# Kernel tuning notes

Measured on AMD Instinct MI355X. Metric: run time of the kernel, lower is better.

The kernel has to match this reference:

```python
import jax, jax.numpy as jnp
import numpy as np

N, K, DIM = 65536, 32, 64


def setup_inputs() -> dict:
    key = jax.random.key(0)
    k1, k2, k3, k4 = jax.random.split(key, 4)
    x = jax.random.normal(k1, (N, DIM), jnp.float32)
    log_pi = jax.random.normal(k2, (K, 1), jnp.float32)
    mu = jax.random.normal(k3, (K, DIM), jnp.float32)
    log_sigma_ = jax.random.normal(k4, (K, DIM, DIM), jnp.float32) / 100.0
    return {"x": x, "log_pi": log_pi, "mu": mu, "log_sigma_": log_sigma_}


def reference(x, log_pi, mu, log_sigma_):
    k, d = mu.shape
    # Faithful to torch: softmax over the size-1 last axis of (K,1) -> all ones.
    pi = jax.nn.softmax(log_pi, axis=-1)  # (K, 1)
    # scale_tril construction: strict lower triangle kept, diagonal -> exp(diag) + 1e-3
    diag = jnp.exp(jnp.diagonal(log_sigma_, axis1=-2, axis2=-1)) + 1e-3  # (K, d)
    L = jnp.tril(log_sigma_, -1) + jnp.eye(d, dtype=x.dtype) * diag[:, None, :]  # (K, d, d)
    # batched MVN log_prob via triangular solve
    diff = x[:, None, :] - mu[None, :, :]            # (N, K, d)
    b = jnp.transpose(diff, (1, 2, 0))               # (K, d, N)
    z = jax.scipy.linalg.solve_triangular(L, b, lower=True)  # (K, d, N)
    maha = jnp.sum(z * z, axis=1)                    # (K, N)
    logdet = jnp.sum(jnp.log(diag), axis=-1)         # (K,)
    logp = -0.5 * (maha + d * jnp.log(2.0 * jnp.pi)) - logdet[:, None]  # (K, N)
    p = jnp.exp(logp).T                              # (N, K)
    return jnp.log(jnp.matmul(p, pi).squeeze())      # (N,)
```

## Files before the change

### kernel.cpp

```cpp
#include <hip/hip_runtime.h>

#define KK 32
#define DD 64
#define NB 65536
#define PAD 68
#define FRAGS 6
#define SLOT (FRAGS * 64)
#define MREF 103.0f
#define L2E 1.4426950408889634f

typedef __attribute__((ext_vector_type(8))) short bf16x8;
typedef __attribute__((ext_vector_type(4))) float f32x4;

__device__ inline short f2bf(float f) {
  uint32_t u = __builtin_bit_cast(uint32_t, f);
  uint32_t r = (u + 0x7fffu + ((u >> 16) & 1u)) >> 16;
  return (short)(r & 0xffffu);
}
__device__ inline uint4 pack8(const short* v) {
  uint4 u;
  u.x = (uint32_t)(unsigned short)v[0] | ((uint32_t)(unsigned short)v[1] << 16);
  u.y = (uint32_t)(unsigned short)v[2] | ((uint32_t)(unsigned short)v[3] << 16);
  u.z = (uint32_t)(unsigned short)v[4] | ((uint32_t)(unsigned short)v[5] << 16);
  u.w = (uint32_t)(unsigned short)v[6] | ((uint32_t)(unsigned short)v[7] << 16);
  return u;
}

__device__ __forceinline__ void gl_lds16(const uint4* g, uint4* l) {
  __builtin_amdgcn_global_load_lds(
      (__attribute__((address_space(1))) void*)g,
      (__attribute__((address_space(3))) void*)l, 16, 0, 0);
}

__global__ __launch_bounds__(256) void md_prep(const float* __restrict__ ls,
                                               const float* __restrict__ mu,
                                               uint4* __restrict__ Bp,
                                               float* __restrict__ Cc,
                                               float* __restrict__ Kcl2) {
  __shared__ float Ls[DD * DD];
  __shared__ float Ys[DD * PAD];
  __shared__ float invdL[DD];
  __shared__ float muL[DD];
  const int k = blockIdx.x, t = threadIdx.x;
  const int j = t >> 2, sub = t & 3;
  const float* __restrict__ lsk = ls + (size_t)k * DD * DD;

#pragma unroll
  for (int it = 0; it < 4; ++it) {
    const int o = (it * 256 + t) * 4;
    *(float4*)&Ls[o] = *(const float4*)&lsk[o];
  }
  if (t < DD) muL[t] = mu[k * DD + t];
  __syncthreads();
  if (t < DD) invdL[t] = 1.0f / (expf(Ls[t * DD + t]) + 1e-3f);
  __syncthreads();

  const float invdj = invdL[j];
  float z[16];
#pragma unroll
  for (int mi = 0; mi < 16; ++mi) z[mi] = 0.f;
#pragma unroll
  for (int i = 0; i < DD; ++i) {
    float p = 0.f;
#pragma unroll
    for (int mi = 0; mi < 16; ++mi) {
      if (4 * mi < i) {
        const int m = 4 * mi + sub;
        p = fmaf(Ls[i * DD + m], (m < i) ? z[mi] : 0.f, p);
      }
    }
    p += __shfl_xor(p, 1, 64);
    p += __shfl_xor(p, 2, 64);
    const float zi = (i == j) ? invdj : -p * invdL[i];
    if (sub == (i & 3)) z[i >> 2] = zi;
  }
#pragma unroll
  for (int mi = 0; mi < 16; ++mi) Ys[(4 * mi + sub) * PAD + j] = z[mi];
  __syncthreads();

  {
    float p = 0.f;
#pragma unroll
    for (int mi = 0; mi < 16; ++mi) {
      const int m = 4 * mi + sub;
      p = fmaf(Ys[j * PAD + m], muL[m], p);
    }
    p += __shfl_xor(p, 1, 64);
    p += __shfl_xor(p, 2, 64);
    if (sub == 0) Cc[k * DD + j] = p;
  }

  if (t < DD) {
    float r = -logf(invdL[t]);
#pragma unroll
    for (int off = 32; off > 0; off >>= 1) r += __shfl_down(r, off, 64);
    if (t == 0)
      Kcl2[k] = (MREF - 0.5f * (64.0f * 1.83787706640934534f) - r) * L2E;
  }

  if (t < DD) {
    const int colp = t & 15, qp = t >> 4;
    uint4* slot = Bp + (size_t)k * SLOT;
#pragma unroll
    for (int s = 0; s < 2; ++s) {
#pragma unroll
      for (int ct = 0; ct < 4; ++ct) {
        if (s == 1 && ct < 2) continue;
        const int i = colp + 16 * ct;
        short hh[8];
#pragma unroll
        for (int jj = 0; jj < 8; ++jj) {
          const int m = s * 32 + qp * 8 + jj;
          const float v = Ys[i * PAD + m] - ((i == m) ? 1.0f : 0.0f);
          hh[jj] = f2bf(v);
        }
        const int fi = (s == 0) ? ct : (2 + ct);
        slot[fi * 64 + t] = pack8(hh);
      }
    }
  }
}

__global__ __launch_bounds__(256, 2) void md_main(const float* __restrict__ x,
                                                  const uint4* __restrict__ Bp,
                                                  const float* __restrict__ Cc,
                                                  const float* __restrict__ Kcl2,
                                                  float* __restrict__ P) {
  __shared__ uint4 lds4[2 * SLOT];
  __shared__ float CcL[8 * DD];
  const int tid = threadIdx.x, lane = tid & 63, w = tid >> 6;
  const int quarter = blockIdx.x & 3;
  const int sblk = blockIdx.x >> 2;
  const int base = sblk * 256 + w * 64;
  const int k0 = quarter * 8;
  const int col = lane & 15, q = lane >> 4;

  bf16x8 Xh[4][2];
#pragma unroll
  for (int Bt = 0; Bt < 4; ++Bt) {
#pragma unroll
    for (int s = 0; s < 2; ++s) {
      const float* src = x + (size_t)(base + Bt * 16 + col) * DD + s * 32 + q * 8;
      const float4 v0 = *(const float4*)src;
      const float4 v1 = *(const float4*)(src + 4);
      const float f[8] = {v0.x, v0.y, v0.z, v0.w, v1.x, v1.y, v1.z, v1.w};
      bf16x8 h;
#pragma unroll
      for (int jj = 0; jj < 8; ++jj) h[jj] = f2bf(f[jj]);
      Xh[Bt][s] = h;
    }
  }

  f32x4 xg[4][4];
#pragma unroll
  for (int ct = 0; ct < 4; ++ct)
#pragma unroll
    for (int Bt = 0; Bt < 4; ++Bt)
      xg[ct][Bt] = *(const f32x4*)&x[(size_t)(base + Bt * 16 + col) * DD +
                                     ct * 16 + q * 4];

  CcL[tid] = Cc[k0 * DD + tid];
  CcL[256 + tid] = Cc[k0 * DD + 256 + tid];

  const int nfr = (w < 2) ? 2 : 1;
  const int fr0 = (w < 2) ? 2 * w : (2 + w);

  {
    const uint4* src = Bp + (size_t)k0 * SLOT;
#pragma unroll
    for (int it = 0; it < 2; ++it)
      if (it < nfr)
        gl_lds16(src + (fr0 + it) * 64 + lane, &lds4[(fr0 + it) * 64]);
  }
  __syncthreads();

  float run_s[4] = {0.f, 0.f, 0.f, 0.f};

#pragma unroll
  for (int kk = 0; kk < 8; ++kk) {
    const int k = k0 + kk;
    const int p = kk & 1;
    if (kk < 7) {
      const uint4* src = Bp + (size_t)(k + 1) * SLOT;
#pragma unroll
      for (int it = 0; it < 2; ++it)
        if (it < nfr)
          gl_lds16(src + (fr0 + it) * 64 + lane,
                   &lds4[(1 - p) * SLOT + (fr0 + it) * 64]);
    }
    const float kc = Kcl2[k];

    const uint4* buf = &lds4[p * SLOT];
    f32x4 mah[4];
#pragma unroll
    for (int Bt = 0; Bt < 4; ++Bt) mah[Bt] = (f32x4){0.f, 0.f, 0.f, 0.f};

#pragma unroll
    for (int ct = 0; ct < 4; ++ct) {
      const bf16x8 A0 = *(const bf16x8*)&buf[ct * 64 + lane];
      bf16x8 A1{};
      if (ct >= 2) A1 = *(const bf16x8*)&buf[(2 + ct) * 64 + lane];
      const f32x4 cK = *(const f32x4*)&CcL[kk * DD + ct * 16 + q * 4];
#pragma unroll
      for (int Bt = 0; Bt < 4; ++Bt) {
        f32x4 z = xg[ct][Bt];
        z = __builtin_amdgcn_mfma_f32_16x16x32_bf16(A0, Xh[Bt][0], z, 0, 0, 0);
        if (ct >= 2)
          z = __builtin_amdgcn_mfma_f32_16x16x32_bf16(A1, Xh[Bt][1], z, 0, 0, 0);
        const f32x4 d = z - cK;
        mah[Bt] += d * d;
      }
    }

#pragma unroll
    for (int Bt = 0; Bt < 4; ++Bt) {
      float s = (mah[Bt][0] + mah[Bt][1]) + (mah[Bt][2] + mah[Bt][3]);
      s += __shfl_xor(s, 16, 64);
      s += __shfl_xor(s, 32, 64);
      const float tt = fmaf(-0.5f * L2E, s, kc);
      run_s[Bt] += exp2f(tt);
    }

    if (kk < 7) __syncthreads();
  }

  if (q == 0) {
#pragma unroll
    for (int Bt = 0; Bt < 4; ++Bt) {
      const int sid = base + Bt * 16 + col;
      P[quarter * NB + sid] = run_s[Bt];
    }
  }
}

__global__ __launch_bounds__(256) void md_comb(const float* __restrict__ P,
                                               float* __restrict__ out) {
  const int n = blockIdx.x * 256 + threadIdx.x;
  const float S = (P[n] + P[NB + n]) + (P[2 * NB + n] + P[3 * NB + n]);
  out[n] = logf(S) - MREF;
}

extern "C" void kernel_launch(void* const* d_in, const int* in_sizes, int n_in,
                              void* d_out, int out_size, void* d_ws, size_t ws_size,
                              hipStream_t stream) {
  const float* x  = (const float*)d_in[0];
  const float* mu = (const float*)d_in[2];
  const float* ls = (const float*)d_in[3];
  float* out = (float*)d_out;

  char* ws = (char*)d_ws;
  uint4* Bp   = (uint4*)ws;
  float* P    = (float*)(ws + (size_t)KK * SLOT * 16);
  float* Cc   = P + 4 * NB;
  float* Kcl2 = Cc + KK * DD;

  md_prep<<<KK, 256, 0, stream>>>(ls, mu, Bp, Cc, Kcl2);
  md_main<<<1024, 256, 0, stream>>>(x, Bp, Cc, Kcl2, P);
  md_comb<<<NB / 256, 256, 0, stream>>>(P, out);
}
```

Baseline: 111.1 us.

## Split mixture components across two blocks and stage two components per barrier

Each md_main block now handles 16 mixture components instead of 8, so the grid shrinks from 1024 to 512 blocks. The x tile is therefore loaded and converted to bf16 half as often, and the partial-sum buffer and combine kernel shrink from four slices to two. The B-matrix prefetch now stages two components per double-buffer step, halving the number of __syncthreads per block. In exchange each block uses twice the LDS, and only 512 blocks are launched, which may reduce occupancy and latency hiding across the device's CUs.

Result: faster. 104.6 us (-5.9%).

```diff
diff --git a/kernel.cpp b/kernel.cpp
--- a/kernel.cpp
+++ b/kernel.cpp
@@ -126,13 +126,13 @@
                                                   const float* __restrict__ Cc,
                                                   const float* __restrict__ Kcl2,
                                                   float* __restrict__ P) {
-  __shared__ uint4 lds4[2 * SLOT];
-  __shared__ float CcL[8 * DD];
+  __shared__ uint4 lds4[4 * SLOT];
+  __shared__ float CcL[16 * DD];
   const int tid = threadIdx.x, lane = tid & 63, w = tid >> 6;
-  const int quarter = blockIdx.x & 3;
-  const int sblk = blockIdx.x >> 2;
+  const int half = blockIdx.x & 1;
+  const int sblk = blockIdx.x >> 1;
   const int base = sblk * 256 + w * 64;
-  const int k0 = quarter * 8;
+  const int k0 = half * 16;
   const int col = lane & 15, q = lane >> 4;
 
   bf16x8 Xh[4][2];
@@ -159,76 +159,78 @@
       xg[ct][Bt] = *(const f32x4*)&x[(size_t)(base + Bt * 16 + col) * DD +
                                      ct * 16 + q * 4];
 
-  CcL[tid] = Cc[k0 * DD + tid];
-  CcL[256 + tid] = Cc[k0 * DD + 256 + tid];
-
-  const int nfr = (w < 2) ? 2 : 1;
-  const int fr0 = (w < 2) ? 2 * w : (2 + w);
-
-  {
-    const uint4* src = Bp + (size_t)k0 * SLOT;
-#pragma unroll
-    for (int it = 0; it < 2; ++it)
-      if (it < nfr)
-        gl_lds16(src + (fr0 + it) * 64 + lane, &lds4[(fr0 + it) * 64]);
+#pragma unroll
+  for (int it = 0; it < 4; ++it)
+    CcL[it * 256 + tid] = Cc[k0 * DD + it * 256 + tid];
+
+#pragma unroll
+  for (int t = 0; t < 3; ++t) {
+    const int f = 3 * w + t, c = f / 6, fi = f % 6;
+    gl_lds16(Bp + (size_t)(k0 + c) * SLOT + fi * 64 + lane,
+             &lds4[c * SLOT + fi * 64]);
   }
   __syncthreads();
 
   float run_s[4] = {0.f, 0.f, 0.f, 0.f};
 
 #pragma unroll
-  for (int kk = 0; kk < 8; ++kk) {
-    const int k = k0 + kk;
-    const int p = kk & 1;
-    if (kk < 7) {
-      const uint4* src = Bp + (size_t)(k + 1) * SLOT;
-#pragma unroll
-      for (int it = 0; it < 2; ++it)
-        if (it < nfr)
-          gl_lds16(src + (fr0 + it) * 64 + lane,
-                   &lds4[(1 - p) * SLOT + (fr0 + it) * 64]);
-    }
-    const float kc = Kcl2[k];
-
-    const uint4* buf = &lds4[p * SLOT];
-    f32x4 mah[4];
-#pragma unroll
-    for (int Bt = 0; Bt < 4; ++Bt) mah[Bt] = (f32x4){0.f, 0.f, 0.f, 0.f};
-
-#pragma unroll
-    for (int ct = 0; ct < 4; ++ct) {
-      const bf16x8 A0 = *(const bf16x8*)&buf[ct * 64 + lane];
-      bf16x8 A1{};
-      if (ct >= 2) A1 = *(const bf16x8*)&buf[(2 + ct) * 64 + lane];
-      const f32x4 cK = *(const f32x4*)&CcL[kk * DD + ct * 16 + q * 4];
+  for (int kp = 0; kp < 8; ++kp) {
+    const int p = kp & 1;
+    if (kp < 7) {
+      const int kb = k0 + 2 * (kp + 1);
+#pragma unroll
+      for (int t = 0; t < 3; ++t) {
+        const int f = 3 * w + t, c = f / 6, fi = f % 6;
+        gl_lds16(Bp + (size_t)(kb + c) * SLOT + fi * 64 + lane,
+                 &lds4[(1 - p) * 2 * SLOT + c * SLOT + fi * 64]);
+      }
+    }
+
+#pragma unroll
+    for (int c = 0; c < 2; ++c) {
+      const int kk = 2 * kp + c;
+      const float kc = Kcl2[k0 + kk];
+      const uint4* buf = &lds4[p * 2 * SLOT + c * SLOT];
+
+      f32x4 mah[4];
+#pragma unroll
+      for (int Bt = 0; Bt < 4; ++Bt) mah[Bt] = (f32x4){0.f, 0.f, 0.f, 0.f};
+
+#pragma unroll
+      for (int ct = 0; ct < 4; ++ct) {
+        const bf16x8 A0 = *(const bf16x8*)&buf[ct * 64 + lane];
+        bf16x8 A1{};
+        if (ct >= 2) A1 = *(const bf16x8*)&buf[(2 + ct) * 64 + lane];
+        const f32x4 cK = *(const f32x4*)&CcL[kk * DD + ct * 16 + q * 4];
+#pragma unroll
+        for (int Bt = 0; Bt < 4; ++Bt) {
+          f32x4 z = xg[ct][Bt];
+          z = __builtin_amdgcn_mfma_f32_16x16x32_bf16(A0, Xh[Bt][0], z, 0, 0, 0);
+          if (ct >= 2)
+            z = __builtin_amdgcn_mfma_f32_16x16x32_bf16(A1, Xh[Bt][1], z, 0, 0, 0);
+          const f32x4 d = z - cK;
+          mah[Bt] += d * d;
+        }
+      }
+
 #pragma unroll
       for (int Bt = 0; Bt < 4; ++Bt) {
-        f32x4 z = xg[ct][Bt];
-        z = __builtin_amdgcn_mfma_f32_16x16x32_bf16(A0, Xh[Bt][0], z, 0, 0, 0);
-        if (ct >= 2)
-          z = __builtin_amdgcn_mfma_f32_16x16x32_bf16(A1, Xh[Bt][1], z, 0, 0, 0);
-        const f32x4 d = z - cK;
-        mah[Bt] += d * d;
-      }
-    }
-
-#pragma unroll
-    for (int Bt = 0; Bt < 4; ++Bt) {
-      float s = (mah[Bt][0] + mah[Bt][1]) + (mah[Bt][2] + mah[Bt][3]);
-      s += __shfl_xor(s, 16, 64);
-      s += __shfl_xor(s, 32, 64);
-      const float tt = fmaf(-0.5f * L2E, s, kc);
-      run_s[Bt] += exp2f(tt);
-    }
-
-    if (kk < 7) __syncthreads();
+        float s = (mah[Bt][0] + mah[Bt][1]) + (mah[Bt][2] + mah[Bt][3]);
+        s += __shfl_xor(s, 16, 64);
+        s += __shfl_xor(s, 32, 64);
+        const float tt = fmaf(-0.5f * L2E, s, kc);
+        run_s[Bt] += exp2f(tt);
+      }
+    }
+
+    if (kp < 7) __syncthreads();
   }
 
   if (q == 0) {
 #pragma unroll
     for (int Bt = 0; Bt < 4; ++Bt) {
       const int sid = base + Bt * 16 + col;
-      P[quarter * NB + sid] = run_s[Bt];
+      P[half * NB + sid] = run_s[Bt];
     }
   }
 }
@@ -236,8 +238,7 @@
 __global__ __launch_bounds__(256) void md_comb(const float* __restrict__ P,
                                                float* __restrict__ out) {
   const int n = blockIdx.x * 256 + threadIdx.x;
-  const float S = (P[n] + P[NB + n]) + (P[2 * NB + n] + P[3 * NB + n]);
-  out[n] = logf(S) - MREF;
+  out[n] = logf(P[n] + P[NB + n]) - MREF;
 }
 
 extern "C" void kernel_launch(void* const* d_in, const int* in_sizes, int n_in,
@@ -251,10 +252,10 @@
   char* ws = (char*)d_ws;
   uint4* Bp   = (uint4*)ws;
   float* P    = (float*)(ws + (size_t)KK * SLOT * 16);
-  float* Cc   = P + 4 * NB;
+  float* Cc   = P + 2 * NB;
   float* Kcl2 = Cc + KK * DD;
 
   md_prep<<<KK, 256, 0, stream>>>(ls, mu, Bp, Cc, Kcl2);
-  md_main<<<1024, 256, 0, stream>>>(x, Bp, Cc, Kcl2, P);
+  md_main<<<512, 256, 0, stream>>>(x, Bp, Cc, Kcl2, P);
   md_comb<<<NB / 256, 256, 0, stream>>>(P, out);
 }
```
